# Kernel tuning notes

Hardware: AMD Instinct MI355X
Metric: run time of the kernel (lower is better)

## Reference

```python
import jax, jax.numpy as jnp
import numpy as np


def setup_inputs() -> dict:
    key = jax.random.key(0)
    ks = jax.random.split(key, 8)
    N, T, U = 8, 200, 50
    E = D = J = 512
    V = 500
    s = lambda k, shape, fan_in: jax.random.normal(k, shape, jnp.float32) / np.sqrt(fan_in)
    return {
        "encoder_out": jax.random.normal(ks[0], (N, T, E), jnp.float32),
        "decoder_out": jax.random.normal(ks[1], (N, U, D), jnp.float32),
        "W_enc": s(ks[2], (J, E), E),
        "b_enc": jax.random.normal(ks[3], (J,), jnp.float32) * 0.01,
        "W_dec": s(ks[4], (J, D), D),
        "b_dec": jax.random.normal(ks[5], (J,), jnp.float32) * 0.01,
        "W_out": s(ks[6], (V, J), J),
        "b_out": jax.random.normal(ks[7], (V,), jnp.float32) * 0.01,
    }


def reference(encoder_out, decoder_out, W_enc, b_enc, W_dec, b_dec, W_out, b_out):
    # Project encoder (N,T,E)->(N,T,J) and decoder (N,U,D)->(N,U,J).
    enc_p = jnp.einsum("nte,je->ntj", encoder_out, W_enc) + b_enc
    dec_p = jnp.einsum("nud,jd->nuj", decoder_out, W_dec) + b_dec
    # Broadcast add -> (N,T,U,J), tanh, then linear to vocab -> (N,T,U,V).
    activations = jnp.tanh(enc_p[:, :, None, :] + dec_p[:, None, :, :])
    logits = jnp.einsum("ntuj,vj->ntuv", activations, W_out) + b_out
    return logits
```

## Files before the change

kernel.cpp:

```cpp
#include <hip/hip_runtime.h>
#include <hip/hip_bf16.h>
#include <stdint.h>

#define JD 512
#define VV 500

typedef short short8 __attribute__((ext_vector_type(8)));
typedef short short4v __attribute__((ext_vector_type(4)));
typedef float floatx4 __attribute__((ext_vector_type(4)));

__device__ inline short f2bf(float f) {
    uint32_t u = __float_as_uint(f);
    uint32_t r = (u + 0x7FFFu + ((u >> 16) & 1u)) >> 16;
    return (short)r;
}

__device__ inline float fast_tanh(float x) {
    float e = __builtin_amdgcn_exp2f(x * 2.8853900817779268f);
    return 1.0f - 2.0f * __builtin_amdgcn_rcpf(e + 1.0f);
}

__global__ __launch_bounds__(256) void prep_kernel(
    const float* __restrict__ Wout, short* __restrict__ WbF)
{
    int j = blockIdx.x * 256 + threadIdx.x;
    int l16 = j & 15;
    int q4  = (j >> 4) & 3;
    int in  = (j >> 6) & 7;
    int wn  = (j >> 9) & 3;
    int ks  = j >> 11;
    int v  = wn * 128 + in * 16 + l16;
    int k0 = ks * 32 + q4 * 8;
    short8 o;
    if (v < VV) {
        const float4* p = (const float4*)(Wout + (size_t)v * JD + k0);
        float4 a = p[0], b = p[1];
        o[0] = f2bf(a.x); o[1] = f2bf(a.y); o[2] = f2bf(a.z); o[3] = f2bf(a.w);
        o[4] = f2bf(b.x); o[5] = f2bf(b.y); o[6] = f2bf(b.z); o[7] = f2bf(b.w);
    } else {
        o = (short8){0,0,0,0,0,0,0,0};
    }
    *(short8*)(WbF + (size_t)j * 8) = o;
}

#define PST 72
__global__ __launch_bounds__(256) void proj_gemm(
    const float* __restrict__ enc, const float* __restrict__ dec,
    const float* __restrict__ Wenc, const float* __restrict__ Wdec,
    const float* __restrict__ b_enc, const float* __restrict__ b_dec,
    float* __restrict__ enc_p, float* __restrict__ dec_p)
{
    __shared__ short As[64 * PST];
    __shared__ short Bs[64 * PST];
    int bx = blockIdx.x, by = blockIdx.y;
    const float* A; const float* W; const float* bias; float* C; int M;
    if (bx < 25) { A = enc; W = Wenc; bias = b_enc; C = enc_p; M = 1600; }
    else { bx -= 25; A = dec; W = Wdec; bias = b_dec; C = dec_p; M = 400; }

    int tid = threadIdx.x;
    int lane = tid & 63, wv = tid >> 6;
    int wm = wv >> 1, wn = wv & 1;
    int l16 = lane & 15, q4 = lane >> 4;

    int ra = tid >> 2, ha = tid & 3;
    int m_st = bx * 64 + ra;
    bool valid = m_st < M;
    int wrow = by * 64 + ra;

    floatx4 acc[2][2];
    #pragma unroll
    for (int a = 0; a < 2; a++)
        #pragma unroll
        for (int b = 0; b < 2; b++) acc[a][b] = (floatx4){0.f, 0.f, 0.f, 0.f};

    for (int kk = 0; kk < 8; kk++) {
        int k0 = kk * 64;
        __syncthreads();
        {
            float4 v0 = make_float4(0.f, 0.f, 0.f, 0.f);
            float4 v1 = v0, v2 = v0, v3 = v0;
            if (valid) {
                const float4* p = (const float4*)(A + (size_t)m_st * JD + k0 + ha * 16);
                v0 = p[0]; v1 = p[1]; v2 = p[2]; v3 = p[3];
            }
            short8 o0, o1;
            o0[0] = f2bf(v0.x); o0[1] = f2bf(v0.y); o0[2] = f2bf(v0.z); o0[3] = f2bf(v0.w);
            o0[4] = f2bf(v1.x); o0[5] = f2bf(v1.y); o0[6] = f2bf(v1.z); o0[7] = f2bf(v1.w);
            o1[0] = f2bf(v2.x); o1[1] = f2bf(v2.y); o1[2] = f2bf(v2.z); o1[3] = f2bf(v2.w);
            o1[4] = f2bf(v3.x); o1[5] = f2bf(v3.y); o1[6] = f2bf(v3.z); o1[7] = f2bf(v3.w);
            *(short8*)&As[ra * PST + ha * 16]     = o0;
            *(short8*)&As[ra * PST + ha * 16 + 8] = o1;

            const float4* pb = (const float4*)(W + (size_t)wrow * JD + k0 + ha * 16);
            float4 w0 = pb[0], w1 = pb[1], w2 = pb[2], w3 = pb[3];
            short8 p0, p1;
            p0[0] = f2bf(w0.x); p0[1] = f2bf(w0.y); p0[2] = f2bf(w0.z); p0[3] = f2bf(w0.w);
            p0[4] = f2bf(w1.x); p0[5] = f2bf(w1.y); p0[6] = f2bf(w1.z); p0[7] = f2bf(w1.w);
            p1[0] = f2bf(w2.x); p1[1] = f2bf(w2.y); p1[2] = f2bf(w2.z); p1[3] = f2bf(w2.w);
            p1[4] = f2bf(w3.x); p1[5] = f2bf(w3.y); p1[6] = f2bf(w3.z); p1[7] = f2bf(w3.w);
            *(short8*)&Bs[ra * PST + ha * 16]     = p0;
            *(short8*)&Bs[ra * PST + ha * 16 + 8] = p1;
        }
        __syncthreads();
        #pragma unroll
        for (int h2 = 0; h2 < 2; h2++) {
            short8 af[2], bf[2];
            #pragma unroll
            for (int im = 0; im < 2; im++)
                af[im] = *(const short8*)&As[(wm * 32 + im * 16 + l16) * PST + h2 * 32 + q4 * 8];
            #pragma unroll
            for (int in = 0; in < 2; in++)
                bf[in] = *(const short8*)&Bs[(wn * 32 + in * 16 + l16) * PST + h2 * 32 + q4 * 8];
            #pragma unroll
            for (int im = 0; im < 2; im++)
                #pragma unroll
                for (int in = 0; in < 2; in++)
                    acc[im][in] = __builtin_amdgcn_mfma_f32_16x16x32_bf16(
                        af[im], bf[in], acc[im][in], 0, 0, 0);
        }
    }
    #pragma unroll
    for (int im = 0; im < 2; im++) {
        int mb = bx * 64 + wm * 32 + im * 16 + q4 * 4;
        #pragma unroll
        for (int rr = 0; rr < 4; rr++) {
            int m = mb + rr;
            if (m < M) {
                #pragma unroll
                for (int in = 0; in < 2; in++) {
                    int j = by * 64 + wn * 32 + in * 16 + l16;
                    C[(size_t)m * JD + j] = acc[im][in][rr] + bias[j];
                }
            }
        }
    }
}

#define AST 520
__global__ __launch_bounds__(512, 4) void fused_joiner(
    const float* __restrict__ enc_p, const float* __restrict__ dec_p,
    const short* __restrict__ WbF, const float* __restrict__ b_out,
    float* __restrict__ out)
{
    __shared__ short As[64 * AST];
    int tid = threadIdx.x;
    int bx = blockIdx.x;

    {
        int rsub = tid >> 7;
        int jf = (tid & 127) * 4;
        #pragma unroll 4
        for (int pass = 0; pass < 16; pass++) {
            int row = pass * 4 + rsub;
            int m = bx * 64 + row;
            int er = m / 50;
            int n  = m / 10000;
            int dr = n * 50 + (m - er * 50);
            float4 e = *(const float4*)(enc_p + (size_t)er * JD + jf);
            float4 d = *(const float4*)(dec_p + (size_t)dr * JD + jf);
            short4v o;
            o[0] = f2bf(fast_tanh(e.x + d.x));
            o[1] = f2bf(fast_tanh(e.y + d.y));
            o[2] = f2bf(fast_tanh(e.z + d.z));
            o[3] = f2bf(fast_tanh(e.w + d.w));
            *(short4v*)&As[row * AST + jf] = o;
        }
    }
    __syncthreads();

    int lane = tid & 63, wv = tid >> 6;
    int wm = wv >> 2, wn = wv & 3;
    int l16 = lane & 15, q4 = lane >> 4;

    floatx4 acc[2][8];
    #pragma unroll
    for (int a = 0; a < 2; a++)
        #pragma unroll
        for (int b = 0; b < 8; b++) acc[a][b] = (floatx4){0.f, 0.f, 0.f, 0.f};

    int abase[2];
    #pragma unroll
    for (int im = 0; im < 2; im++)
        abase[im] = (wm * 32 + im * 16 + l16) * AST + q4 * 8;

    const short* wp = WbF + wn * 4096 + q4 * 128 + l16 * 8;

    for (int ks = 0; ks < 16; ks++) {
        short8 bfr[8];
        #pragma unroll
        for (int in = 0; in < 8; in++)
            bfr[in] = *(const short8*)(wp + in * 512);
        short8 af[2];
        int k0 = ks * 32;
        #pragma unroll
        for (int im = 0; im < 2; im++)
            af[im] = *(const short8*)&As[abase[im] + k0];
        #pragma unroll
        for (int im = 0; im < 2; im++)
            #pragma unroll
            for (int in = 0; in < 8; in++)
                acc[im][in] = __builtin_amdgcn_mfma_f32_16x16x32_bf16(
                    af[im], bfr[in], acc[im][in], 0, 0, 0);
        wp += 16384;
    }

    float bo[8];
    #pragma unroll
    for (int in = 0; in < 8; in++) {
        int v = wn * 128 + in * 16 + l16;
        bo[in] = (v < VV) ? b_out[v] : 0.f;
    }
    #pragma unroll
    for (int im = 0; im < 2; im++) {
        int mb = bx * 64 + wm * 32 + im * 16 + q4 * 4;
        #pragma unroll
        for (int rr = 0; rr < 4; rr++) {
            size_t orow = (size_t)(mb + rr) * VV;
            #pragma unroll
            for (int in = 0; in < 8; in++) {
                int v = wn * 128 + in * 16 + l16;
                if (v < VV)
                    __builtin_nontemporal_store(acc[im][in][rr] + bo[in],
                                                &out[orow + v]);
            }
        }
    }
}

extern "C" void kernel_launch(void* const* d_in, const int* in_sizes, int n_in,
                              void* d_out, int out_size, void* d_ws, size_t ws_size,
                              hipStream_t stream)
{
    const float* enc   = (const float*)d_in[0];
    const float* dec   = (const float*)d_in[1];
    const float* Wenc  = (const float*)d_in[2];
    const float* b_enc = (const float*)d_in[3];
    const float* Wdec  = (const float*)d_in[4];
    const float* b_dec = (const float*)d_in[5];
    const float* Wout  = (const float*)d_in[6];
    const float* b_out = (const float*)d_in[7];
    float* out = (float*)d_out;

    char* ws = (char*)d_ws;
    short* WbF   = (short*)(ws + 0);
    float* enc_p = (float*)(ws + 524288);
    float* dec_p = (float*)(ws + 3801088);

    prep_kernel<<<128, 256, 0, stream>>>(Wout, WbF);
    proj_gemm<<<dim3(32, 8), 256, 0, stream>>>(enc, dec, Wenc, Wdec,
                                               b_enc, b_dec, enc_p, dec_p);
    fused_joiner<<<1250, 512, 0, stream>>>(enc_p, dec_p, WbF, b_out, out);
}
```

Baseline: 257.1 us.

## Keep W_out slices register-resident in persistent joiner blocks iterating over row tiles

The joiner becomes a 125x2 grid of persistent blocks. Each block loads its 256-column slice of bf16 W_out into registers once, then loops over 10 row tiles, computing tanh activations into double-buffered LDS and running MFMAs against the resident weights. This removes the repeated per-tile global/L2 reads of W_out. In exchange each block recomputes the activations for both vocab halves, register pressure rises, occupancy drops, the grid is much smaller, and output stores are no longer nontemporal.

```diff
diff --git a/kernel.cpp b/kernel.cpp
--- a/kernel.cpp
+++ b/kernel.cpp
@@ -137,22 +137,50 @@
 }
 
 #define AST 520
-__global__ __launch_bounds__(512, 4) void fused_joiner(
+__global__ __launch_bounds__(512, 2) void fused_joiner(
     const float* __restrict__ enc_p, const float* __restrict__ dec_p,
     const short* __restrict__ WbF, const float* __restrict__ b_out,
     float* __restrict__ out)
 {
-    __shared__ short As[64 * AST];
+    __shared__ short As[2][64 * AST];
     int tid = threadIdx.x;
-    int bx = blockIdx.x;
-
+    int mgrp = blockIdx.x;
+    int vg   = blockIdx.y;
+    int lane = tid & 63, wv = tid >> 6;
+    int l16 = lane & 15, q4 = lane >> 4;
+
+    int wn  = vg * 2 + (wv >> 2);
+    int in0 = (wv & 3) * 2;
+    int vb0 = wn * 128 + in0 * 16;
+
+    short8 breg0[16], breg1[16];
     {
-        int rsub = tid >> 7;
-        int jf = (tid & 127) * 4;
+        const short* bp = WbF + q4 * 128 + l16 * 8 + (wn * 8 + in0) * 512;
+        #pragma unroll
+        for (int ks = 0; ks < 16; ks++) {
+            breg0[ks] = *(const short8*)(bp + ks * 16384);
+            breg1[ks] = *(const short8*)(bp + ks * 16384 + 512);
+        }
+    }
+
+    float bo0, bo1;
+    {
+        int v0 = vb0 + l16, v1 = vb0 + 16 + l16;
+        bo0 = (v0 < VV) ? b_out[v0] : 0.f;
+        bo1 = (v1 < VV) ? b_out[v1] : 0.f;
+    }
+
+    int rsub = tid >> 7;
+    int jf   = (tid & 127) * 4;
+
+    for (int t = 0; t < 10; t++) {
+        int m0 = (mgrp * 10 + t) * 64;
+        short* buf = &As[t & 1][0];
+
         #pragma unroll 4
         for (int pass = 0; pass < 16; pass++) {
             int row = pass * 4 + rsub;
-            int m = bx * 64 + row;
+            int m = m0 + row;
             int er = m / 50;
             int n  = m / 10000;
             int dr = n * 50 + (m - er * 50);
@@ -163,65 +191,27 @@
             o[1] = f2bf(fast_tanh(e.y + d.y));
             o[2] = f2bf(fast_tanh(e.z + d.z));
             o[3] = f2bf(fast_tanh(e.w + d.w));
-            *(short4v*)&As[row * AST + jf] = o;
-        }
-    }
-    __syncthreads();
-
-    int lane = tid & 63, wv = tid >> 6;
-    int wm = wv >> 2, wn = wv & 3;
-    int l16 = lane & 15, q4 = lane >> 4;
-
-    floatx4 acc[2][8];
-    #pragma unroll
-    for (int a = 0; a < 2; a++)
-        #pragma unroll
-        for (int b = 0; b < 8; b++) acc[a][b] = (floatx4){0.f, 0.f, 0.f, 0.f};
-
-    int abase[2];
-    #pragma unroll
-    for (int im = 0; im < 2; im++)
-        abase[im] = (wm * 32 + im * 16 + l16) * AST + q4 * 8;
-
-    const short* wp = WbF + wn * 4096 + q4 * 128 + l16 * 8;
-
-    for (int ks = 0; ks < 16; ks++) {
-        short8 bfr[8];
-        #pragma unroll
-        for (int in = 0; in < 8; in++)
-            bfr[in] = *(const short8*)(wp + in * 512);
-        short8 af[2];
-        int k0 = ks * 32;
-        #pragma unroll
-        for (int im = 0; im < 2; im++)
-            af[im] = *(const short8*)&As[abase[im] + k0];
-        #pragma unroll
-        for (int im = 0; im < 2; im++)
-            #pragma unroll
-            for (int in = 0; in < 8; in++)
-                acc[im][in] = __builtin_amdgcn_mfma_f32_16x16x32_bf16(
-                    af[im], bfr[in], acc[im][in], 0, 0, 0);
-        wp += 16384;
-    }
-
-    float bo[8];
-    #pragma unroll
-    for (int in = 0; in < 8; in++) {
-        int v = wn * 128 + in * 16 + l16;
-        bo[in] = (v < VV) ? b_out[v] : 0.f;
-    }
-    #pragma unroll
-    for (int im = 0; im < 2; im++) {
-        int mb = bx * 64 + wm * 32 + im * 16 + q4 * 4;
-        #pragma unroll
-        for (int rr = 0; rr < 4; rr++) {
-            size_t orow = (size_t)(mb + rr) * VV;
-            #pragma unroll
-            for (int in = 0; in < 8; in++) {
-                int v = wn * 128 + in * 16 + l16;
-                if (v < VV)
-                    __builtin_nontemporal_store(acc[im][in][rr] + bo[in],
-                                                &out[orow + v]);
+            *(short4v*)&buf[row * AST + jf] = o;
+        }
+        __syncthreads();
+
+        #pragma unroll
+        for (int ms = 0; ms < 4; ms++) {
+            int ab = (ms * 16 + l16) * AST + q4 * 8;
+            floatx4 a0 = (floatx4){0.f, 0.f, 0.f, 0.f};
+            floatx4 a1 = (floatx4){0.f, 0.f, 0.f, 0.f};
+            #pragma unroll
+            for (int ks = 0; ks < 16; ks++) {
+                short8 af = *(const short8*)&buf[ab + ks * 32];
+                a0 = __builtin_amdgcn_mfma_f32_16x16x32_bf16(af, breg0[ks], a0, 0, 0, 0);
+                a1 = __builtin_amdgcn_mfma_f32_16x16x32_bf16(af, breg1[ks], a1, 0, 0, 0);
+            }
+            int v0 = vb0 + l16, v1 = vb0 + 16 + l16;
+            #pragma unroll
+            for (int rr = 0; rr < 4; rr++) {
+                size_t orow = (size_t)(m0 + ms * 16 + q4 * 4 + rr) * VV;
+                if (v0 < VV) out[orow + v0] = a0[rr] + bo0;
+                if (v1 < VV) out[orow + v1] = a1[rr] + bo1;
             }
         }
     }
@@ -249,5 +239,5 @@
     prep_kernel<<<128, 256, 0, stream>>>(Wout, WbF);
     proj_gemm<<<dim3(32, 8), 256, 0, stream>>>(enc, dec, Wenc, Wdec,
                                                b_enc, b_dec, enc_p, dec_p);
-    fused_joiner<<<1250, 512, 0, stream>>>(enc_p, dec_p, WbF, b_out, out);
-}
+    fused_joiner<<<dim3(125, 2), 512, 0, stream>>>(enc_p, dec_p, WbF, b_out, out);
+}
```

Result: faster. 238.3 us (-7.3%).
